# Kernel optimization log

Hardware: AMD Instinct MI355X
Metric: run time of the kernel (lower is better)

Reference implementation:

```python
import jax, jax.numpy as jnp
import numpy as np

IN_DIM = 1024
MEM = 1024
N = 2048  # number of tree nodes (chain: parent of node i is node i-1)


def setup_inputs() -> dict:
    key = jax.random.key(0)
    ks = jax.random.split(key, 11)
    s_in = 1.0 / np.sqrt(IN_DIM)
    s_m = 1.0 / np.sqrt(MEM)

    def u(k, shape, s):
        return jax.random.uniform(k, shape, jnp.float32, -s, s)

    return {
        "inputs": jax.random.normal(ks[0], (N, IN_DIM), jnp.float32),
        "Wx": u(ks[1], (IN_DIM, 5 * MEM), s_in),   # iofzux weight (transposed vs torch)
        "bx": u(ks[2], (5 * MEM,), s_in),
        "Wh": u(ks[3], (MEM, 4 * MEM), s_m),        # iofzh weight
        "bh": u(ks[4], (4 * MEM,), s_m),
        "Wum": u(ks[5], (MEM, MEM), s_m),           # um weight
        "bum": u(ks[6], (MEM,), s_m),
        "pic": u(ks[7], (MEM,), s_m),               # CMul peephole weights
        "pfc": u(ks[8], (MEM,), s_m),
        "poc": u(ks[9], (MEM,), s_m),
        "pzc": u(ks[10], (MEM,), s_m),
    }


def reference(inputs, Wx, bx, Wh, bh, Wum, bum, pic, pfc, poc, pzc):
    # Precompute the input projection for all nodes at once (same math,
    # just batched): torch split order is i, o, f, z, u.
    Gx = inputs @ Wx + bx                      # (N, 5*MEM)
    ix, ox, fx, zx, ux = jnp.split(Gx, 5, axis=1)

    def step(carry, g):
        c_p, h_p = carry                       # parent cell / hidden, (MEM,)
        gix, gox, gfx, gzx, gux = g
        gh = h_p @ Wh + bh                     # (4*MEM,)
        ih, oh, fh, zh = jnp.split(gh, 4)
        i = jax.nn.sigmoid(gix + ih + pic * c_p)
        f = jax.nn.sigmoid(gfx + fh + pfc * c_p)
        z = jax.nn.sigmoid(gzx + zh + pzc * c_p)
        u = jnp.tanh(gux + (z * jnp.tanh(c_p)) @ Wum + bum)
        c = i * u + f * c_p
        o = jax.nn.sigmoid(gox + oh + poc * c)  # peephole on o uses new c
        h = o * jnp.tanh(c)
        return (c, h), h

    zero = jnp.zeros((MEM,), jnp.float32)
    _, hs = jax.lax.scan(step, (zero, zero), (ix, ox, fx, zx, ux))  # hs: (N, MEM)
    # forward() concatenates all node h states and takes elementwise max
    return jnp.max(hs, axis=0, keepdims=True)  # (1, MEM)
```

## Files before the change

### kernel.cpp

```cpp
#include <hip/hip_runtime.h>
#include <math.h>

#define IN_DIM 1024
#define MEM 1024
#define NNODE 2048
#define GX_COLS 5120

#define NWG 128
#define WGT 512
#define DPW 8
#define PUBI (NWG * 16)

__device__ __forceinline__ float fsig(float x) {
  return __builtin_amdgcn_rcpf(1.f + __expf(-x));
}
__device__ __forceinline__ float ftanh(float x) {
  return 1.f - 2.f * __builtin_amdgcn_rcpf(1.f + __expf(2.f * x));
}

__device__ __forceinline__ void store_pair(int* p, float v, int tg) {
  int2 d; d.x = __float_as_int(v); d.y = tg;
  asm volatile("global_store_dwordx2 %0, %1, off sc0 sc1"
               :: "v"(p), "v"(d) : "memory");
}
__device__ __forceinline__ void poll_pairs(const int* p, int tg,
                                           float4& lo, float4& hi) {
  int4 a, b, c, d;
  do {
    asm volatile(
        "global_load_dwordx4 %0, %4, off sc0 sc1\n\t"
        "global_load_dwordx4 %1, %4, off offset:16 sc0 sc1\n\t"
        "global_load_dwordx4 %2, %4, off offset:32 sc0 sc1\n\t"
        "global_load_dwordx4 %3, %4, off offset:48 sc0 sc1\n\t"
        "s_waitcnt vmcnt(0)"
        : "=v"(a), "=v"(b), "=v"(c), "=v"(d)
        : "v"(p) : "memory");
  } while ((a.y ^ tg) | (a.w ^ tg) | (b.y ^ tg) | (b.w ^ tg) |
           (c.y ^ tg) | (c.w ^ tg) | (d.y ^ tg) | (d.w ^ tg));
  lo = make_float4(__int_as_float(a.x), __int_as_float(a.z),
                   __int_as_float(b.x), __int_as_float(b.z));
  hi = make_float4(__int_as_float(c.x), __int_as_float(c.z),
                   __int_as_float(d.x), __int_as_float(d.z));
}

__global__ void init_ctrl(int* h_pub, int* v_pub) {
  int t = threadIdx.x;
  for (int i = t; i < PUBI / 2; i += blockDim.x) {
    h_pub[2 * i + 0] = 0;
    h_pub[2 * i + 1] = 0;
  }
  for (int i = t; i < PUBI / 2; i += blockDim.x) {
    h_pub[PUBI + 2 * i + 0] = 0;
    h_pub[PUBI + 2 * i + 1] = -1;
  }
  for (int i = t; i < PUBI; i += blockDim.x) {
    v_pub[2 * i + 0] = 0;
    v_pub[2 * i + 1] = -1;
  }
}

__global__ __launch_bounds__(256) void gemm_gx(
    const float* __restrict__ A, const float* __restrict__ B,
    const float* __restrict__ bias, float* __restrict__ C) {
  __shared__ float As[8][128];
  __shared__ float Bs[8][132];
  const int tid = threadIdx.x;
  const int bm = blockIdx.y * 128;
  const int bn = blockIdx.x * 128;
  const int tx = tid & 15;
  const int ty = tid >> 4;
  const int am = tid >> 1;
  const int ak = (tid & 1) * 4;
  const int bk = tid >> 5;
  const int bn4 = (tid & 31) * 4;

  float acc[8][8] = {};
  for (int k0 = 0; k0 < IN_DIM; k0 += 8) {
    float4 av = *(const float4*)&A[(size_t)(bm + am) * IN_DIM + k0 + ak];
    float4 bv = *(const float4*)&B[(size_t)(k0 + bk) * GX_COLS + bn + bn4];
    __syncthreads();
    As[ak + 0][am] = av.x;
    As[ak + 1][am] = av.y;
    As[ak + 2][am] = av.z;
    As[ak + 3][am] = av.w;
    *(float4*)&Bs[bk][bn4] = bv;
    __syncthreads();
#pragma unroll
    for (int kk = 0; kk < 8; ++kk) {
      float4 a0 = *(const float4*)&As[kk][ty * 4];
      float4 a1 = *(const float4*)&As[kk][64 + ty * 4];
      float4 b0 = *(const float4*)&Bs[kk][tx * 4];
      float4 b1 = *(const float4*)&Bs[kk][64 + tx * 4];
      float a[8] = {a0.x, a0.y, a0.z, a0.w, a1.x, a1.y, a1.z, a1.w};
      float b[8] = {b0.x, b0.y, b0.z, b0.w, b1.x, b1.y, b1.z, b1.w};
#pragma unroll
      for (int i = 0; i < 8; ++i)
#pragma unroll
        for (int j = 0; j < 8; ++j) acc[i][j] += a[i] * b[j];
    }
  }
  float4 bias0 = *(const float4*)&bias[bn + tx * 4];
  float4 bias1 = *(const float4*)&bias[bn + 64 + tx * 4];
#pragma unroll
  for (int i = 0; i < 8; ++i) {
    int row = bm + ((i < 4) ? (ty * 4 + i) : (64 + ty * 4 + (i - 4)));
    float4 c0 = {acc[i][0] + bias0.x, acc[i][1] + bias0.y,
                 acc[i][2] + bias0.z, acc[i][3] + bias0.w};
    float4 c1 = {acc[i][4] + bias1.x, acc[i][5] + bias1.y,
                 acc[i][6] + bias1.z, acc[i][7] + bias1.w};
    *(float4*)&C[(size_t)row * GX_COLS + bn + tx * 4] = c0;
    *(float4*)&C[(size_t)row * GX_COLS + bn + 64 + tx * 4] = c1;
  }
}

__global__ __launch_bounds__(WGT) void scan_kernel(
    const float* __restrict__ Wh, const float* __restrict__ bh,
    const float* __restrict__ Wum, const float* __restrict__ bum,
    const float* __restrict__ pic, const float* __restrict__ pfc,
    const float* __restrict__ poc, const float* __restrict__ pzc,
    const float* __restrict__ Gx,
    int* h_pub, int* v_pub,
    float* __restrict__ out) {
  const int wg = blockIdx.x;
  const int tid = threadIdx.x;
  const int w = tid >> 6;
  const int ln = tid & 63;
  const int j = wg * DPW + w;
  const bool leader = (ln == 0);

  __shared__ float h_lds[MEM];
  __shared__ float v_lds[MEM];
  __shared__ float share[DPW];

  float wi[16], wo[16], wf[16], wz[16], wu[16];
#pragma unroll
  for (int m = 0; m < 4; ++m)
#pragma unroll
    for (int e = 0; e < 4; ++e) {
      int k = ln * 4 + m * 256 + e;
      wi[m * 4 + e] = Wh[(size_t)k * 4096 + 0 * MEM + j];
      wo[m * 4 + e] = Wh[(size_t)k * 4096 + 1 * MEM + j];
      wf[m * 4 + e] = Wh[(size_t)k * 4096 + 2 * MEM + j];
      wz[m * 4 + e] = Wh[(size_t)k * 4096 + 3 * MEM + j];
      wu[m * 4 + e] = Wum[(size_t)k * MEM + j];
    }

  float b_i = 0, b_o = 0, b_f = 0, b_z = 0, b_u = 0;
  float p_i = 0, p_f = 0, p_o = 0, p_z = 0;
  if (leader) {
    b_i = bh[0 * MEM + j]; b_o = bh[1 * MEM + j];
    b_f = bh[2 * MEM + j]; b_z = bh[3 * MEM + j];
    b_u = bum[j];
    p_i = pic[j]; p_f = pfc[j]; p_o = poc[j]; p_z = pzc[j];
  }

  float g_i = 0, g_o = 0, g_f = 0, g_z = 0, g_u = 0;
  float n_i = 0, n_o = 0, n_f = 0, n_z = 0, n_u = 0;
  if (leader) {
    g_i = Gx[j];           g_o = Gx[MEM + j];     g_f = Gx[2 * MEM + j];
    g_z = Gx[3 * MEM + j]; g_u = Gx[4 * MEM + j];
  }

  float c = 0.f, hmax = -1e30f;
  float i_keep = 0, f_keep = 0, oh_keep = 0, gux_keep = 0;

  for (int t = 0; t < NNODE; ++t) {
    if (leader && t + 1 < NNODE) {
      const float* gx = Gx + (size_t)(t + 1) * GX_COLS;
      n_i = gx[j];           n_o = gx[MEM + j];     n_f = gx[2 * MEM + j];
      n_z = gx[3 * MEM + j]; n_u = gx[4 * MEM + j];
    }

    if (tid >= 64 && tid < 192) {
      const int idx = tid - 64;
      float4 lo, hi;
      poll_pairs(h_pub + (t & 1) * PUBI + idx * 16, t, lo, hi);
      *(float4*)&h_lds[idx * 8] = lo;
      *(float4*)&h_lds[idx * 8 + 4] = hi;
    }
    __syncthreads();

    float hreg[16];
#pragma unroll
    for (int m = 0; m < 4; ++m) {
      float4 hv = *(const float4*)&h_lds[m * 256 + ln * 4];
      hreg[m * 4 + 0] = hv.x; hreg[m * 4 + 1] = hv.y;
      hreg[m * 4 + 2] = hv.z; hreg[m * 4 + 3] = hv.w;
    }

    float sz = 0;
#pragma unroll
    for (int q = 0; q < 16; ++q) sz += hreg[q] * wz[q];
#pragma unroll
    for (int off = 32; off >= 1; off >>= 1) sz += __shfl_down(sz, off);
    if (leader) {
      float zv = fsig(g_z + sz + b_z + p_z * c);
      share[w] = zv * ftanh(c);
    }
    __syncthreads();

    if (tid < 8)
      store_pair(v_pub + (t & 1) * PUBI + wg * 16 + tid * 2, share[tid], t + 1);

    float si = 0, so = 0, sf = 0;
#pragma unroll
    for (int q = 0; q < 16; ++q) {
      si += hreg[q] * wi[q]; so += hreg[q] * wo[q]; sf += hreg[q] * wf[q];
    }
#pragma unroll
    for (int off = 32; off >= 1; off >>= 1) {
      si += __shfl_down(si, off); so += __shfl_down(so, off);
      sf += __shfl_down(sf, off);
    }
    if (leader) {
      i_keep = fsig(g_i + si + b_i + p_i * c);
      f_keep = fsig(g_f + sf + b_f + p_f * c);
      oh_keep = g_o + so + b_o;
      gux_keep = g_u;
    }

    if (tid >= 192 && tid < 320) {
      const int idx = tid - 192;
      float4 lo, hi;
      poll_pairs(v_pub + (t & 1) * PUBI + idx * 16, t + 1, lo, hi);
      *(float4*)&v_lds[idx * 8] = lo;
      *(float4*)&v_lds[idx * 8 + 4] = hi;
    }
    __syncthreads();

    float sm = 0;
#pragma unroll
    for (int m = 0; m < 4; ++m) {
      float4 vv4 = *(const float4*)&v_lds[m * 256 + ln * 4];
      const float* vv = (const float*)&vv4;
#pragma unroll
      for (int e = 0; e < 4; ++e) sm += vv[e] * wu[m * 4 + e];
    }
#pragma unroll
    for (int off = 32; off >= 1; off >>= 1) sm += __shfl_down(sm, off);
    if (leader) {
      float uv = ftanh(gux_keep + sm + b_u);
      float cn = i_keep * uv + f_keep * c;
      float ov = fsig(oh_keep + p_o * cn);
      float hn = ov * ftanh(cn);
      c = cn;
      hmax = fmaxf(hmax, hn);
      share[w] = hn;
      g_i = n_i; g_o = n_o; g_f = n_f; g_z = n_z; g_u = n_u;
    }
    __syncthreads();

    if (tid < 8)
      store_pair(h_pub + ((t + 1) & 1) * PUBI + wg * 16 + tid * 2,
                 share[tid], t + 1);
  }

  if (leader) out[j] = hmax;
}

extern "C" void kernel_launch(void* const* d_in, const int* in_sizes, int n_in,
                              void* d_out, int out_size, void* d_ws, size_t ws_size,
                              hipStream_t stream) {
  const float* inputs = (const float*)d_in[0];
  const float* Wx  = (const float*)d_in[1];
  const float* bx  = (const float*)d_in[2];
  const float* Wh  = (const float*)d_in[3];
  const float* bh  = (const float*)d_in[4];
  const float* Wum = (const float*)d_in[5];
  const float* bum = (const float*)d_in[6];
  const float* pic = (const float*)d_in[7];
  const float* pfc = (const float*)d_in[8];
  const float* poc = (const float*)d_in[9];
  const float* pzc = (const float*)d_in[10];
  float* out = (float*)d_out;

  float* Gx = (float*)d_ws;
  int* h_pub = (int*)(Gx + (size_t)NNODE * GX_COLS);
  int* v_pub = h_pub + 2 * PUBI;

  init_ctrl<<<1, 256, 0, stream>>>(h_pub, v_pub);
  gemm_gx<<<dim3(GX_COLS / 128, NNODE / 128), 256, 0, stream>>>(inputs, Wx, bx, Gx);
  scan_kernel<<<NWG, WGT, 0, stream>>>(Wh, bh, Wum, bum, pic, pfc, poc, pzc,
                                       Gx, h_pub, v_pub, out);
}
```

Measured before the change: 7.014 ms.

## Halve scan workgroups by assigning two hidden units per wavefront

```diff
diff --git a/kernel.cpp b/kernel.cpp
--- a/kernel.cpp
+++ b/kernel.cpp
@@ -6,10 +6,10 @@
 #define NNODE 2048
 #define GX_COLS 5120
 
-#define NWG 128
+#define NWG 64
 #define WGT 512
-#define DPW 8
-#define PUBI (NWG * 16)
+#define DPW 16
+#define PUBI (NWG * DPW * 2)
 
 __device__ __forceinline__ float fsig(float x) {
   return __builtin_amdgcn_rcpf(1.f + __expf(-x));
@@ -125,19 +125,21 @@
   const int tid = threadIdx.x;
   const int w = tid >> 6;
   const int ln = tid & 63;
-  const int j = wg * DPW + w;
-  const bool leader = (ln == 0);
+  const int half = ln >> 5;
+  const int lh = ln & 31;
+  const int j = wg * DPW + 2 * w + half;
+  const bool leader = (lh == 0);
 
   __shared__ float h_lds[MEM];
   __shared__ float v_lds[MEM];
   __shared__ float share[DPW];
 
-  float wi[16], wo[16], wf[16], wz[16], wu[16];
-#pragma unroll
-  for (int m = 0; m < 4; ++m)
+  float wi[32], wo[32], wf[32], wz[32], wu[32];
+#pragma unroll
+  for (int m = 0; m < 8; ++m)
 #pragma unroll
     for (int e = 0; e < 4; ++e) {
-      int k = ln * 4 + m * 256 + e;
+      int k = lh * 4 + m * 128 + e;
       wi[m * 4 + e] = Wh[(size_t)k * 4096 + 0 * MEM + j];
       wo[m * 4 + e] = Wh[(size_t)k * 4096 + 1 * MEM + j];
       wf[m * 4 + e] = Wh[(size_t)k * 4096 + 2 * MEM + j];
@@ -180,37 +182,37 @@
     }
     __syncthreads();
 
-    float hreg[16];
-#pragma unroll
-    for (int m = 0; m < 4; ++m) {
-      float4 hv = *(const float4*)&h_lds[m * 256 + ln * 4];
+    float hreg[32];
+#pragma unroll
+    for (int m = 0; m < 8; ++m) {
+      float4 hv = *(const float4*)&h_lds[m * 128 + lh * 4];
       hreg[m * 4 + 0] = hv.x; hreg[m * 4 + 1] = hv.y;
       hreg[m * 4 + 2] = hv.z; hreg[m * 4 + 3] = hv.w;
     }
 
     float sz = 0;
 #pragma unroll
-    for (int q = 0; q < 16; ++q) sz += hreg[q] * wz[q];
-#pragma unroll
-    for (int off = 32; off >= 1; off >>= 1) sz += __shfl_down(sz, off);
+    for (int q = 0; q < 32; ++q) sz += hreg[q] * wz[q];
+#pragma unroll
+    for (int off = 16; off >= 1; off >>= 1) sz += __shfl_down(sz, off, 32);
     if (leader) {
       float zv = fsig(g_z + sz + b_z + p_z * c);
-      share[w] = zv * ftanh(c);
-    }
-    __syncthreads();
-
-    if (tid < 8)
-      store_pair(v_pub + (t & 1) * PUBI + wg * 16 + tid * 2, share[tid], t + 1);
+      share[2 * w + half] = zv * ftanh(c);
+    }
+    __syncthreads();
+
+    if (tid < DPW)
+      store_pair(v_pub + (t & 1) * PUBI + wg * 32 + tid * 2, share[tid], t + 1);
 
     float si = 0, so = 0, sf = 0;
 #pragma unroll
-    for (int q = 0; q < 16; ++q) {
+    for (int q = 0; q < 32; ++q) {
       si += hreg[q] * wi[q]; so += hreg[q] * wo[q]; sf += hreg[q] * wf[q];
     }
 #pragma unroll
-    for (int off = 32; off >= 1; off >>= 1) {
-      si += __shfl_down(si, off); so += __shfl_down(so, off);
-      sf += __shfl_down(sf, off);
+    for (int off = 16; off >= 1; off >>= 1) {
+      si += __shfl_down(si, off, 32); so += __shfl_down(so, off, 32);
+      sf += __shfl_down(sf, off, 32);
     }
     if (leader) {
       i_keep = fsig(g_i + si + b_i + p_i * c);
@@ -230,14 +232,13 @@
 
     float sm = 0;
 #pragma unroll
-    for (int m = 0; m < 4; ++m) {
-      float4 vv4 = *(const float4*)&v_lds[m * 256 + ln * 4];
-      const float* vv = (const float*)&vv4;
-#pragma unroll
-      for (int e = 0; e < 4; ++e) sm += vv[e] * wu[m * 4 + e];
-    }
-#pragma unroll
-    for (int off = 32; off >= 1; off >>= 1) sm += __shfl_down(sm, off);
+    for (int m = 0; m < 8; ++m) {
+      float4 vv4 = *(const float4*)&v_lds[m * 128 + lh * 4];
+      sm += vv4.x * wu[m * 4 + 0] + vv4.y * wu[m * 4 + 1] +
+            vv4.z * wu[m * 4 + 2] + vv4.w * wu[m * 4 + 3];
+    }
+#pragma unroll
+    for (int off = 16; off >= 1; off >>= 1) sm += __shfl_down(sm, off, 32);
     if (leader) {
       float uv = ftanh(gux_keep + sm + b_u);
       float cn = i_keep * uv + f_keep * c;
@@ -245,13 +246,13 @@
       float hn = ov * ftanh(cn);
       c = cn;
       hmax = fmaxf(hmax, hn);
-      share[w] = hn;
+      share[2 * w + half] = hn;
       g_i = n_i; g_o = n_o; g_f = n_f; g_z = n_z; g_u = n_u;
     }
     __syncthreads();
 
-    if (tid < 8)
-      store_pair(h_pub + ((t + 1) & 1) * PUBI + wg * 16 + tid * 2,
+    if (tid < DPW)
+      store_pair(h_pub + ((t + 1) & 1) * PUBI + wg * 32 + tid * 2,
                  share[tid], t + 1);
   }
 
```

New measurement: 6.883 ms. No clear change (-1.9%).
